# Performance work log

Measured on AMD Instinct MI355X. Metric: run time of the kernel, lower is better.

Reference implementation:

```python
import jax, jax.numpy as jnp
import numpy as np

DIM = 64
HEADS = 1
SR = 8
EPS = 1e-5


def layer_norm(x, g, b):
    mu = jnp.mean(x, axis=-1, keepdims=True)
    var = jnp.var(x, axis=-1, keepdims=True)
    return (x - mu) * jax.lax.rsqrt(var + EPS) * g + b


def setup_inputs() -> dict:
    key = jax.random.key(0)
    ks = jax.random.split(key, 10)
    B, N, C = 8, 16384, DIM
    s = 1.0 / np.sqrt(C)
    return {
        "x": jax.random.normal(ks[0], (B, N, C), dtype=jnp.float32),
        "H": 128,
        "W": 128,
        "Wq": jax.random.normal(ks[1], (C, C), dtype=jnp.float32) * s,
        "bq": jnp.zeros((C,), jnp.float32),
        "Wkv": jax.random.normal(ks[2], (C, 2 * C), dtype=jnp.float32) * s,
        "bkv": jnp.zeros((2 * C,), jnp.float32),
        "sr_w": jax.random.normal(ks[3], (C, C, SR, SR), dtype=jnp.float32) * (1.0 / np.sqrt(C * SR * SR)),
        "sr_b": jnp.zeros((C,), jnp.float32),
        "ln_g": jnp.ones((C,), jnp.float32),
        "ln_b": jnp.zeros((C,), jnp.float32),
        "Wp": jax.random.normal(ks[4], (C, C), dtype=jnp.float32) * s,
        "bp": jnp.zeros((C,), jnp.float32),
    }


def reference(x, H, W, Wq, bq, Wkv, bkv, sr_w, sr_b, ln_g, ln_b, Wp, bp):
    B, N, C = x.shape
    h, d = HEADS, C // HEADS
    scale = d ** -0.5
    # Q at full resolution: [B, h, N, d]
    q = (x @ Wq + bq).reshape(B, N, h, d).transpose(0, 2, 1, 3)
    # Spatial reduction: conv(k=SR, stride=SR) then LayerNorm
    x2d = x.transpose(0, 2, 1).reshape(B, C, H, W)
    x2d = jax.lax.conv_general_dilated(
        x2d, sr_w, window_strides=(SR, SR), padding="VALID",
        dimension_numbers=("NCHW", "OIHW", "NCHW")) + sr_b[None, :, None, None]
    xr = x2d.reshape(B, C, -1).transpose(0, 2, 1)  # [B, Nk, C]
    xr = layer_norm(xr, ln_g, ln_b)
    # K, V on reduced sequence: [B, h, Nk, d]
    kv = (xr @ Wkv + bkv).reshape(B, -1, 2, h, d).transpose(2, 0, 3, 1, 4)
    k, v = kv[0], kv[1]
    # attn_drop(p=0) is identity; softmax over Nk
    attn = jax.nn.softmax(jnp.einsum("bhnd,bhkd->bhnk", q, k) * scale, axis=-1)
    out = jnp.einsum("bhnk,bhkd->bhnd", attn, v).transpose(0, 2, 1, 3).reshape(B, N, C)
    return out @ Wp + bp
```

## Files before the change

kernel.cpp:

```cpp
#include <hip/hip_runtime.h>
#include <hip/hip_bf16.h>
#include <hip/hip_fp16.h>
#include <math.h>


#define B 8
#define N 16384
#define C 64
#define NK 256
#define HW 128

typedef unsigned short ushort_t;
typedef unsigned int uint_t;
typedef __attribute__((ext_vector_type(8))) short short8v;
typedef __attribute__((ext_vector_type(16))) float f32x16;

static __device__ inline ushort_t f2bf(float f) {
  __hip_bfloat16 h = __float2bfloat16(f);
  return *reinterpret_cast<ushort_t*>(&h);
}
static __device__ inline uint_t cvtpk(float a, float b) {
  uint_t r;
  asm("v_cvt_pk_bf16_f32 %0, %1, %2" : "=v"(r) : "v"(a), "v"(b));
  return r;
}
static __device__ inline uint_t pkh(float a, float b) {
  auto h2 = __builtin_amdgcn_cvt_pkrtz(a, b);
  return *reinterpret_cast<uint_t*>(&h2);
}
static __device__ inline float uf16lo(uint_t v) {
  ushort_t s = (ushort_t)v;
  _Float16 h = *reinterpret_cast<_Float16*>(&s);
  return (float)h;
}
static __device__ inline float uf16hi(uint_t v) {
  ushort_t s = (ushort_t)(v >> 16);
  _Float16 h = *reinterpret_cast<_Float16*>(&s);
  return (float)h;
}
static __device__ inline short8v mk8(uint_t a, uint_t b, uint_t c, uint_t d) {
  union { int4 i; short8v s; } u;
  u.i = make_int4((int)a, (int)b, (int)c, (int)d);
  return u.s;
}
static __device__ inline float sum16(const f32x16 v) {
  float a = ((v[0] + v[1]) + (v[2] + v[3])) + ((v[4] + v[5]) + (v[6] + v[7]));
  float b = ((v[8] + v[9]) + (v[10] + v[11])) + ((v[12] + v[13]) + (v[14] + v[15]));
  return a + b;
}

__global__ __launch_bounds__(256) void prep0(
    const float* __restrict__ sr_w, const float* __restrict__ Wq,
    const float* __restrict__ Wkv, const float* __restrict__ bq,
    const float* __restrict__ Wp, const float* __restrict__ bkv,
    const float* __restrict__ bp, ushort_t* __restrict__ Wf,
    ushort_t* __restrict__ W2f, float* __restrict__ u,
    float* __restrict__ bp2) {
  const int bid = blockIdx.x;
  const int t = threadIdx.x;
  const float SC = 0.125f * 1.4426950408889634f;
  if (bid < 1024) {
    int idx = bid * 256 + t;
    int o = idx >> 12;
    int r = idx & 4095;
    int c = r >> 6;
    int ki = (r >> 3) & 7;
    int kj = r & 7;
    int oh = o >> 5;
    int l = ((c >> 3) & 1) * 32 + (o & 31);
    int kk = kj * 4 + (c >> 4);
    int e = c & 7;
    Wf[(ki * 2 + oh) * 16384 + kk * 512 + l * 8 + e] = f2bf(sr_w[idx]);
  } else if (bid < 1040) {
    const int eb = bid - 1024;
#pragma unroll
    for (int q = 0; q < 2; ++q) {
      int oidx = eb * 512 + t * 2 + q;
      int mat = oidx >> 12;
      int rem = oidx & 4095;
      int d = rem >> 6;
      int c = rem & 63;
      float s = 0.f;
      if (mat == 0) {
        const float* wk = Wkv + d * 128;
        const float* wq = Wq + c * 64;
#pragma unroll 16
        for (int e = 0; e < 64; ++e) s += wk[e] * wq[e];
        s *= SC;
      } else {
        const float* wk = Wkv + d * 128 + 64;
#pragma unroll 16
        for (int e = 0; e < 64; ++e) s += wk[e] * Wp[e * 64 + c];
      }
      W2f[((mat * 2 + (c >> 5)) * 4 + (d >> 4)) * 512 +
          (((d >> 3) & 1) * 32 + (c & 31)) * 8 + (d & 7)] = f2bf(s);
    }
  } else {
    if (t < 64) {
      float s = 0.f;
      const float* wk = Wkv + t * 128;
#pragma unroll 16
      for (int e = 0; e < 64; ++e) s += wk[e] * bq[e];
      u[t] = s * SC;
    } else if (t < 128) {
      int c = t - 64;
      float s = bp[c];
#pragma unroll 16
      for (int e = 0; e < 64; ++e) s += bkv[64 + e] * Wp[e * 64 + c];
      bp2[c] = s;
    }
  }
}

__global__ __launch_bounds__(128) void conv_mfma(
    const float* __restrict__ x, const ushort_t* __restrict__ Wf,
    ushort_t* __restrict__ parth) {
  const int t = threadIdx.x;
  const int bi = blockIdx.x;
  const int ki = bi & 7;
  const int pg = (bi >> 3) & 7;
  const int b = (bi >> 6) & 7;
  const int half = bi >> 9;
  const int oh = t >> 6;
  const int lane = t & 63;
  const int lo5 = lane & 31;
  const int hi = lane >> 5;

  const int P = pg * 32 + lo5;
  const int prow = P >> 4, pcol = P & 15;
  const float* rowbase =
      x + ((size_t)b * N + (prow * 8 + ki) * HW + pcol * 8) * C;
  const ushort_t* wbase = Wf + (ki * 2 + oh) * 16384 + lane * 8;

  f32x16 acc;
#pragma unroll
  for (int r = 0; r < 16; ++r) acc[r] = 0.f;

#pragma unroll
  for (int kkl = 0; kkl < 16; ++kkl) {
    const int kk = half * 16 + kkl;
    const int kj = kk >> 2;
    const int c0 = (kk & 3) * 16 + hi * 8;
    const float4* xp = reinterpret_cast<const float4*>(rowbase + kj * C + c0);
    float4 f0 = xp[0];
    float4 f1 = xp[1];
    short8v bfr = mk8(cvtpk(f0.x, f0.y), cvtpk(f0.z, f0.w), cvtpk(f1.x, f1.y),
                      cvtpk(f1.z, f1.w));
    short8v afr = *reinterpret_cast<const short8v*>(wbase + kk * 512);
    acc = __builtin_amdgcn_mfma_f32_32x32x16_bf16(afr, bfr, acc, 0, 0, 0);
  }

  ushort_t* dst = parth + (size_t)bi * 2048 + oh * 1024 + lane * 16;
  uint4 v0 = make_uint4(pkh(acc[0], acc[1]), pkh(acc[2], acc[3]),
                        pkh(acc[4], acc[5]), pkh(acc[6], acc[7]));
  uint4 v1 = make_uint4(pkh(acc[8], acc[9]), pkh(acc[10], acc[11]),
                        pkh(acc[12], acc[13]), pkh(acc[14], acc[15]));
  *reinterpret_cast<uint4*>(dst) = v0;
  *reinterpret_cast<uint4*>(dst + 8) = v1;
}

__global__ __launch_bounds__(256) void ln_prep(
    const ushort_t* __restrict__ parth, const float* __restrict__ sr_b,
    const float* __restrict__ ln_g, const float* __restrict__ ln_b,
    const ushort_t* __restrict__ W2f, const float* __restrict__ u,
    ushort_t* __restrict__ MTf, ushort_t* __restrict__ VpTf,
    ushort_t* __restrict__ sbf) {
  __shared__ float convs[32 * 68];
  __shared__ float ns[32 * 68];

  const int t = threadIdx.x;
  const int b = blockIdx.x >> 3;
  const int pg = blockIdx.x & 7;
  const size_t obase = (size_t)b * 16384;

  {
    const int lane = t & 63;
    const int rhalf = (t >> 6) & 1;
    const int oh = t >> 7;
    float a[8];
#pragma unroll
    for (int r = 0; r < 8; ++r) a[r] = 0.f;
#pragma unroll
    for (int k2 = 0; k2 < 16; ++k2) {
      int bi = (k2 & 7) + (pg << 3) + (b << 6) + ((k2 >> 3) << 9);
      const ushort_t* src =
          parth + (size_t)bi * 2048 + oh * 1024 + lane * 16 + rhalf * 8;
      uint4 uv = *reinterpret_cast<const uint4*>(src);
      a[0] += uf16lo(uv.x); a[1] += uf16hi(uv.x);
      a[2] += uf16lo(uv.y); a[3] += uf16hi(uv.y);
      a[4] += uf16lo(uv.z); a[5] += uf16hi(uv.z);
      a[6] += uf16lo(uv.w); a[7] += uf16hi(uv.w);
    }
    const int p = lane & 31;
#pragma unroll
    for (int r = 0; r < 8; ++r) {
      int reg = rhalf * 8 + r;
      int o = oh * 32 + (reg & 3) + 8 * (reg >> 2) + 4 * (lane >> 5);
      convs[p * 68 + o] = a[r] + sr_b[o];
    }
  }
  __syncthreads();
  {
    const int lane = t & 63;
    const int w = t >> 6;
    float g = ln_g[lane], bb = ln_b[lane];
#pragma unroll
    for (int rr = 0; rr < 8; ++rr) {
      int p = w * 8 + rr;
      float v = convs[p * 68 + lane];
      float s = v, s2 = v * v;
#pragma unroll
      for (int mask = 1; mask < 64; mask <<= 1) {
        s += __shfl_xor(s, mask, 64);
        s2 += __shfl_xor(s2, mask, 64);
      }
      float mu = s * (1.f / 64.f);
      float var = s2 * (1.f / 64.f) - mu * mu;
      ns[p * 68 + lane] = (v - mu) * rsqrtf(var + 1e-5f) * g + bb;
    }
  }
  __syncthreads();
  {
    const int w = t >> 6;
    const int lane = t & 63;
    const int lo5 = lane & 31;
    const int hi = lane >> 5;
    const int mat = w >> 1;
    const int n0 = w & 1;

    f32x16 acc;
#pragma unroll
    for (int r = 0; r < 16; ++r) acc[r] = 0.f;
#pragma unroll
    for (int ks = 0; ks < 4; ++ks) {
      float4 f0 = *reinterpret_cast<const float4*>(&ns[lo5 * 68 + ks * 16 + hi * 8]);
      float4 f1 = *reinterpret_cast<const float4*>(&ns[lo5 * 68 + ks * 16 + hi * 8 + 4]);
      short8v A = mk8(cvtpk(f0.x, f0.y), cvtpk(f0.z, f0.w), cvtpk(f1.x, f1.y),
                      cvtpk(f1.z, f1.w));
      short8v Bw = *reinterpret_cast<const short8v*>(
          W2f + ((mat * 2 + n0) * 4 + ks) * 512 + lane * 8);
      acc = __builtin_amdgcn_mfma_f32_32x32x16_bf16(A, Bw, acc, 0, 0, 0);
    }
    const int c = n0 * 32 + lo5;
    if (mat == 0) {
#pragma unroll
      for (int r = 0; r < 16; ++r) {
        int jl = (r & 3) + 8 * (r >> 2) + 4 * hi;
        MTf[obase + (pg * 4 + (c >> 4)) * 512 +
            (((c >> 3) & 1) * 32 + jl) * 8 + (c & 7)] = f2bf(acc[r]);
      }
    } else {
#pragma unroll
      for (int r = 0; r < 16; ++r) {
        int jg = pg * 32 + (r & 3) + 8 * (r >> 2) + 4 * hi;
        VpTf[obase + (n0 * 16 + (jg >> 4)) * 512 +
             (((jg >> 3) & 1) * 32 + (c & 31)) * 8 + (jg & 7)] = f2bf(acc[r]);
      }
    }
    if (w == 0) {
      float s = 0.f;
      const float* ub = u + hi * 32;
#pragma unroll 8
      for (int dd = 0; dd < 32; ++dd) s += ns[lo5 * 68 + hi * 32 + dd] * ub[dd];
      s += __shfl_xor(s, 32, 64);
      if (hi == 0) sbf[b * NK + pg * 32 + lo5] = f2bf(s);
    }
  }
}

__global__ __launch_bounds__(256, 4) void attn_mfma(
    const float* __restrict__ x, const ushort_t* __restrict__ MTf,
    const ushort_t* __restrict__ VpTf, const ushort_t* __restrict__ sbf,
    const float* __restrict__ bp2, float* __restrict__ outp) {
  __shared__ __align__(16) char smem[34816 + 512];
  ushort_t* sMT = reinterpret_cast<ushort_t*>(smem);
  float* sOut = reinterpret_cast<float*>(smem);
  ushort_t* sSB = reinterpret_cast<ushort_t*>(smem + 34816);

  const int t = threadIdx.x;
  const int b = blockIdx.x >> 7;
  const int qb = blockIdx.x & 127;
  const int wave = t >> 6;
  const int lane = t & 63;
  const int lo5 = lane & 31;
  const int hi = lane >> 5;

  const int row = qb * 128 + wave * 32 + lo5;
  const float4* xp =
      reinterpret_cast<const float4*>(x + ((size_t)b * N + row) * 64);
  float4 xf[8];
#pragma unroll
  for (int ks = 0; ks < 4; ++ks) {
    xf[2 * ks + 0] = xp[ks * 4 + hi * 2 + 0];
    xf[2 * ks + 1] = xp[ks * 4 + hi * 2 + 1];
  }

  {
    const uint4* gm = reinterpret_cast<const uint4*>(MTf + (size_t)b * 16384);
    uint4* dm = reinterpret_cast<uint4*>(sMT);
#pragma unroll
    for (int i = 0; i < 8; ++i) dm[t + i * 256] = gm[t + i * 256];
    if (t < 32)
      reinterpret_cast<uint4*>(sSB)[t] =
          reinterpret_cast<const uint4*>(sbf + b * NK)[t];
  }
  __syncthreads();

  short8v bx[4];
#pragma unroll
  for (int ks = 0; ks < 4; ++ks) {
    bx[ks] = mk8(cvtpk(xf[2 * ks].x, xf[2 * ks].y),
                 cvtpk(xf[2 * ks].z, xf[2 * ks].w),
                 cvtpk(xf[2 * ks + 1].x, xf[2 * ks + 1].y),
                 cvtpk(xf[2 * ks + 1].z, xf[2 * ks + 1].w));
  }

  const ushort_t* vt = VpTf + (size_t)b * 16384 + lane * 8;

  f32x16 zv;
#pragma unroll
  for (int r = 0; r < 16; ++r) zv[r] = 0.f;

  f32x16 o[2];
#pragma unroll
  for (int ct = 0; ct < 2; ++ct)
#pragma unroll
    for (int r = 0; r < 16; ++r) o[ct][r] = 0.f;
  float sum = 0.f;

#pragma unroll 1
  for (int kt2 = 0; kt2 < 4; ++kt2) {
    const int kta = kt2 * 2;
    const int ktb = kta + 1;
    __builtin_amdgcn_s_setprio(1);
    const short8v afa0 =
        *reinterpret_cast<const short8v*>(&sMT[(kta * 4 + 0) * 512 + lane * 8]);
    const short8v afb0 =
        *reinterpret_cast<const short8v*>(&sMT[(ktb * 4 + 0) * 512 + lane * 8]);
    f32x16 a0 = __builtin_amdgcn_mfma_f32_32x32x16_bf16(afa0, bx[0], zv, 0, 0, 0);
    f32x16 a1 = __builtin_amdgcn_mfma_f32_32x32x16_bf16(afb0, bx[0], zv, 0, 0, 0);
#pragma unroll
    for (int ks = 1; ks < 4; ++ks) {
      const short8v aa =
          *reinterpret_cast<const short8v*>(&sMT[(kta * 4 + ks) * 512 + lane * 8]);
      const short8v ab =
          *reinterpret_cast<const short8v*>(&sMT[(ktb * 4 + ks) * 512 + lane * 8]);
      a0 = __builtin_amdgcn_mfma_f32_32x32x16_bf16(aa, bx[ks], a0, 0, 0, 0);
      a1 = __builtin_amdgcn_mfma_f32_32x32x16_bf16(ab, bx[ks], a1, 0, 0, 0);
    }
    {
      ushort_t sva = sSB[kta * 32 + lo5];
      ushort_t svb = sSB[ktb * 32 + lo5];
      short8v b5 = mk8(hi ? 0u : 0x3F80u, 0u, 0u, 0u);
      short8v a5a = mk8(hi ? 0u : (uint_t)sva, 0u, 0u, 0u);
      short8v a5b = mk8(hi ? 0u : (uint_t)svb, 0u, 0u, 0u);
      a0 = __builtin_amdgcn_mfma_f32_32x32x16_bf16(a5a, b5, a0, 0, 0, 0);
      a1 = __builtin_amdgcn_mfma_f32_32x32x16_bf16(a5b, b5, a1, 0, 0, 0);
    }
    __builtin_amdgcn_s_setprio(0);
#pragma unroll
    for (int r = 0; r < 16; ++r) a0[r] = __builtin_amdgcn_exp2f(a0[r]);
#pragma unroll
    for (int r = 0; r < 16; ++r) a1[r] = __builtin_amdgcn_exp2f(a1[r]);
    sum += sum16(a0) + sum16(a1);
#pragma unroll
    for (int ph = 0; ph < 4; ++ph) {
      const int kt = (ph < 2) ? kta : ktb;
      const int m0 = (ph & 1) * 2;
      const f32x16& av = (ph < 2) ? a0 : a1;
      uint_t Aw = cvtpk(av[4 * m0 + 0], av[4 * m0 + 1]);
      uint_t Bw = cvtpk(av[4 * m0 + 2], av[4 * m0 + 3]);
      uint_t Cw = cvtpk(av[4 * m0 + 4], av[4 * m0 + 5]);
      uint_t Dw = cvtpk(av[4 * m0 + 6], av[4 * m0 + 7]);
      asm volatile("v_permlane32_swap_b32 %0, %1" : "+v"(Aw), "+v"(Cw));
      asm volatile("v_permlane32_swap_b32 %0, %1" : "+v"(Bw), "+v"(Dw));
      const short8v pb = mk8(Aw, Bw, Cw, Dw);
      const int kss = kt * 2 + (ph & 1);
      __builtin_amdgcn_s_setprio(1);
#pragma unroll
      for (int ct = 0; ct < 2; ++ct) {
        const short8v va =
            *reinterpret_cast<const short8v*>(vt + (ct * 16 + kss) * 512);
        o[ct] = __builtin_amdgcn_mfma_f32_32x32x16_bf16(va, pb, o[ct], 0, 0, 0);
      }
      __builtin_amdgcn_s_setprio(0);
    }
  }

  sum += __shfl_xor(sum, 32, 64);
  const float linv = 1.f / sum;

  __syncthreads();
  {
    float* wout = sOut + wave * 2176;
#pragma unroll
    for (int ct = 0; ct < 2; ++ct) {
#pragma unroll
      for (int g = 0; g < 4; ++g) {
        int c0 = ct * 32 + g * 8 + hi * 4;
        float4 bpv = *reinterpret_cast<const float4*>(bp2 + c0);
        float4 r;
        r.x = o[ct][4 * g + 0] * linv + bpv.x;
        r.y = o[ct][4 * g + 1] * linv + bpv.y;
        r.z = o[ct][4 * g + 2] * linv + bpv.z;
        r.w = o[ct][4 * g + 3] * linv + bpv.w;
        *reinterpret_cast<float4*>(&wout[lo5 * 68 + c0]) = r;
      }
    }
  }
  __syncthreads();
  {
    float* outBase = outp + (((size_t)b * N + qb * 128) * 64);
#pragma unroll
    for (int qi = 0; qi < 8; ++qi) {
      int rowl = qi * 16 + (t >> 4);
      int c4 = (t & 15) * 4;
      float4 v = *reinterpret_cast<const float4*>(
          &sOut[(rowl >> 5) * 2176 + (rowl & 31) * 68 + c4]);
      *reinterpret_cast<float4*>(outBase + qi * 1024 + t * 4) = v;
    }
  }
}

extern "C" void kernel_launch(void* const* d_in, const int* in_sizes, int n_in,
                              void* d_out, int out_size, void* d_ws,
                              size_t ws_size, hipStream_t stream) {
  const float* x    = (const float*)d_in[0];
  const float* Wq   = (const float*)d_in[3];
  const float* bq   = (const float*)d_in[4];
  const float* Wkv  = (const float*)d_in[5];
  const float* bkv  = (const float*)d_in[6];
  const float* sr_w = (const float*)d_in[7];
  const float* sr_b = (const float*)d_in[8];
  const float* ln_g = (const float*)d_in[9];
  const float* ln_b = (const float*)d_in[10];
  const float* Wp   = (const float*)d_in[11];
  const float* bp   = (const float*)d_in[12];
  float* outp = (float*)d_out;

  char* ws = (char*)d_ws;
  ushort_t* Wf    = (ushort_t*)(ws);
  ushort_t* W2f   = (ushort_t*)(ws + (512 << 10));
  float*    u     = (float*)(ws + (528 << 10));
  float*    bp2   = (float*)(ws + (528 << 10) + 256);
  ushort_t* parth = (ushort_t*)(ws + (1024 << 10));
  ushort_t* MTf   = (ushort_t*)(ws + (9216 << 10));
  ushort_t* VpTf  = (ushort_t*)(ws + (9472 << 10));
  ushort_t* sbf   = (ushort_t*)(ws + (9728 << 10));

  prep0<<<1041, 256, 0, stream>>>(sr_w, Wq, Wkv, bq, Wp, bkv, bp, Wf, W2f, u, bp2);
  conv_mfma<<<1024, 128, 0, stream>>>(x, Wf, parth);
  ln_prep<<<64, 256, 0, stream>>>(parth, sr_b, ln_g, ln_b, W2f, u, MTf, VpTf, sbf);
  attn_mfma<<<1024, 256, 0, stream>>>(x, MTf, VpTf, sbf, bp2, outp);
}
```

Measured before the change: 49.49 us.

## Stage V tiles into LDS with double-buffered async global_load_lds

Instead of every wave reading V fragments straight from global memory in the PV loop, the block cooperatively copies each V key-tile pair into one of two LDS buffers with global_load_lds, prefetching the next tile while the current one is consumed. The softmax bias values are now read directly from global memory instead of being copied into LDS. The aim is to cut the fourfold redundant global/L2 traffic for V and hide its latency behind the MFMA work. In exchange it adds two block-wide barriers per iteration and raises LDS use to 40 KB, which may limit how much the waves can overlap.

```diff
diff --git a/kernel.cpp b/kernel.cpp
--- a/kernel.cpp
+++ b/kernel.cpp
@@ -272,10 +272,11 @@
     const float* __restrict__ x, const ushort_t* __restrict__ MTf,
     const ushort_t* __restrict__ VpTf, const ushort_t* __restrict__ sbf,
     const float* __restrict__ bp2, float* __restrict__ outp) {
-  __shared__ __align__(16) char smem[34816 + 512];
+  __shared__ __align__(16) char smem[40960];
   ushort_t* sMT = reinterpret_cast<ushort_t*>(smem);
+  ushort_t* sVPa = reinterpret_cast<ushort_t*>(smem + 32768);
+  ushort_t* sVPb = reinterpret_cast<ushort_t*>(smem + 36864);
   float* sOut = reinterpret_cast<float*>(smem);
-  ushort_t* sSB = reinterpret_cast<ushort_t*>(smem + 34816);
 
   const int t = threadIdx.x;
   const int b = blockIdx.x >> 7;
@@ -285,6 +286,18 @@
   const int lo5 = lane & 31;
   const int hi = lane >> 5;
 
+  const ushort_t* vtb = VpTf + (size_t)b * 16384;
+  const ushort_t* sbg = sbf + b * NK;
+
+  auto stage = [&](int kt, ushort_t* buf) {
+    const int ct = t >> 7;
+    const ushort_t* src = vtb + (ct * 16 + kt * 2) * 512 + (t & 127) * 8;
+    __builtin_amdgcn_global_load_lds(
+        (const __attribute__((address_space(1))) unsigned int*)src,
+        (__attribute__((address_space(3))) unsigned int*)(buf + wave * 512),
+        16, 0, 0);
+  };
+
   const int row = qb * 128 + wave * 32 + lo5;
   const float4* xp =
       reinterpret_cast<const float4*>(x + ((size_t)b * N + row) * 64);
@@ -300,9 +313,7 @@
     uint4* dm = reinterpret_cast<uint4*>(sMT);
 #pragma unroll
     for (int i = 0; i < 8; ++i) dm[t + i * 256] = gm[t + i * 256];
-    if (t < 32)
-      reinterpret_cast<uint4*>(sSB)[t] =
-          reinterpret_cast<const uint4*>(sbf + b * NK)[t];
+    stage(0, sVPa);
   }
   __syncthreads();
 
@@ -315,8 +326,6 @@
                  cvtpk(xf[2 * ks + 1].z, xf[2 * ks + 1].w));
   }
 
-  const ushort_t* vt = VpTf + (size_t)b * 16384 + lane * 8;
-
   f32x16 zv;
 #pragma unroll
   for (int r = 0; r < 16; ++r) zv[r] = 0.f;
@@ -332,6 +341,9 @@
   for (int kt2 = 0; kt2 < 4; ++kt2) {
     const int kta = kt2 * 2;
     const int ktb = kta + 1;
+    ushort_t sva = sbg[kta * 32 + lo5];
+    ushort_t svb = sbg[ktb * 32 + lo5];
+    stage(ktb, sVPb);
     __builtin_amdgcn_s_setprio(1);
     const short8v afa0 =
         *reinterpret_cast<const short8v*>(&sMT[(kta * 4 + 0) * 512 + lane * 8]);
@@ -349,8 +361,6 @@
       a1 = __builtin_amdgcn_mfma_f32_32x32x16_bf16(ab, bx[ks], a1, 0, 0, 0);
     }
     {
-      ushort_t sva = sSB[kta * 32 + lo5];
-      ushort_t svb = sSB[ktb * 32 + lo5];
       short8v b5 = mk8(hi ? 0u : 0x3F80u, 0u, 0u, 0u);
       short8v a5a = mk8(hi ? 0u : (uint_t)sva, 0u, 0u, 0u);
       short8v a5b = mk8(hi ? 0u : (uint_t)svb, 0u, 0u, 0u);
@@ -364,33 +374,51 @@
     for (int r = 0; r < 16; ++r) a1[r] = __builtin_amdgcn_exp2f(a1[r]);
     sum += sum16(a0) + sum16(a1);
 #pragma unroll
-    for (int ph = 0; ph < 4; ++ph) {
-      const int kt = (ph < 2) ? kta : ktb;
-      const int m0 = (ph & 1) * 2;
-      const f32x16& av = (ph < 2) ? a0 : a1;
-      uint_t Aw = cvtpk(av[4 * m0 + 0], av[4 * m0 + 1]);
-      uint_t Bw = cvtpk(av[4 * m0 + 2], av[4 * m0 + 3]);
-      uint_t Cw = cvtpk(av[4 * m0 + 4], av[4 * m0 + 5]);
-      uint_t Dw = cvtpk(av[4 * m0 + 6], av[4 * m0 + 7]);
+    for (int ph = 0; ph < 2; ++ph) {
+      const int m0 = ph * 2;
+      uint_t Aw = cvtpk(a0[4 * m0 + 0], a0[4 * m0 + 1]);
+      uint_t Bw = cvtpk(a0[4 * m0 + 2], a0[4 * m0 + 3]);
+      uint_t Cw = cvtpk(a0[4 * m0 + 4], a0[4 * m0 + 5]);
+      uint_t Dw = cvtpk(a0[4 * m0 + 6], a0[4 * m0 + 7]);
       asm volatile("v_permlane32_swap_b32 %0, %1" : "+v"(Aw), "+v"(Cw));
       asm volatile("v_permlane32_swap_b32 %0, %1" : "+v"(Bw), "+v"(Dw));
       const short8v pb = mk8(Aw, Bw, Cw, Dw);
-      const int kss = kt * 2 + (ph & 1);
       __builtin_amdgcn_s_setprio(1);
 #pragma unroll
       for (int ct = 0; ct < 2; ++ct) {
-        const short8v va =
-            *reinterpret_cast<const short8v*>(vt + (ct * 16 + kss) * 512);
+        const short8v va = *reinterpret_cast<const short8v*>(
+            &sVPa[ct * 1024 + ph * 512 + lane * 8]);
         o[ct] = __builtin_amdgcn_mfma_f32_32x32x16_bf16(va, pb, o[ct], 0, 0, 0);
       }
       __builtin_amdgcn_s_setprio(0);
     }
+    __syncthreads();
+    if (kt2 < 3) stage(kta + 2, sVPa);
+#pragma unroll
+    for (int ph = 0; ph < 2; ++ph) {
+      const int m0 = ph * 2;
+      uint_t Aw = cvtpk(a1[4 * m0 + 0], a1[4 * m0 + 1]);
+      uint_t Bw = cvtpk(a1[4 * m0 + 2], a1[4 * m0 + 3]);
+      uint_t Cw = cvtpk(a1[4 * m0 + 4], a1[4 * m0 + 5]);
+      uint_t Dw = cvtpk(a1[4 * m0 + 6], a1[4 * m0 + 7]);
+      asm volatile("v_permlane32_swap_b32 %0, %1" : "+v"(Aw), "+v"(Cw));
+      asm volatile("v_permlane32_swap_b32 %0, %1" : "+v"(Bw), "+v"(Dw));
+      const short8v pb = mk8(Aw, Bw, Cw, Dw);
+      __builtin_amdgcn_s_setprio(1);
+#pragma unroll
+      for (int ct = 0; ct < 2; ++ct) {
+        const short8v va = *reinterpret_cast<const short8v*>(
+            &sVPb[ct * 1024 + ph * 512 + lane * 8]);
+        o[ct] = __builtin_amdgcn_mfma_f32_32x32x16_bf16(va, pb, o[ct], 0, 0, 0);
+      }
+      __builtin_amdgcn_s_setprio(0);
+    }
+    __syncthreads();
   }
 
   sum += __shfl_xor(sum, 32, 64);
   const float linv = 1.f / sum;
 
-  __syncthreads();
   {
     float* wout = sOut + wave * 2176;
 #pragma unroll
```

Result: no change. 49.97 us (+1.0%).
